# Kernel optimization log

Measured on AMD Instinct MI355X. Metric: run time of the kernel, lower is better.

## Reference

```python
import jax, jax.numpy as jnp
import numpy as np

D_K = 64
D_MODEL = 1024
N_HEADS = 16


def setup_inputs() -> dict:
    key = jax.random.key(0)
    ks = jax.random.split(key, 9)
    B, S = 2, 2048
    scale = 1.0 / np.sqrt(D_MODEL)
    inp = {
        "x": jax.random.normal(ks[0], (B, S, D_MODEL), dtype=jnp.float32),
        "w_q": jax.random.normal(ks[1], (D_MODEL, N_HEADS * D_K), dtype=jnp.float32) * scale,
        "b_q": jnp.zeros((N_HEADS * D_K,), dtype=jnp.float32),
        "w_k": jax.random.normal(ks[2], (D_MODEL, N_HEADS * D_K), dtype=jnp.float32) * scale,
        "b_k": jnp.zeros((N_HEADS * D_K,), dtype=jnp.float32),
        "w_v": jax.random.normal(ks[3], (D_MODEL, N_HEADS * D_K), dtype=jnp.float32) * scale,
        "b_v": jnp.zeros((N_HEADS * D_K,), dtype=jnp.float32),
        "w_o": jax.random.normal(ks[4], (N_HEADS * D_K, D_MODEL), dtype=jnp.float32) * scale,
        "b_o": jnp.zeros((D_MODEL,), dtype=jnp.float32),
    }
    return inp


def reference(x, w_q, b_q, w_k, b_k, w_v, b_v, w_o, b_o):
    B, S, _ = x.shape
    H, Dk = N_HEADS, D_K

    def split_heads(m):  # [B,S,H*Dk] -> [B,H,S,Dk]
        return m.reshape(B, S, H, Dk).transpose(0, 2, 1, 3)

    Q = split_heads(x @ w_q + b_q)
    K = split_heads(x @ w_k + b_k)
    V = split_heads(x @ w_v + b_v)

    scores = jnp.einsum("bhsd,bhtd->bhst", Q, K) / jnp.sqrt(jnp.float32(Dk))
    probs = jax.nn.softmax(scores, axis=-1)
    attn = jnp.einsum("bhst,bhtd->bhsd", probs, V)  # [B,H,S,Dk]
    attn = attn.transpose(0, 2, 1, 3).reshape(B, S, H * Dk)
    return attn @ w_o + b_o
```

## Files before the change

### kernel.cpp

```cpp
#include <hip/hip_runtime.h>
#include <math.h>

#define D_MODELc 1024
#define N_HEADSc 16
#define D_Kc     64
#define B_SZc    2
#define S_LENc   2048
#define NTOKc    (B_SZc * S_LENc)
#define SPLITc   4

using half8  = __attribute__((ext_vector_type(8))) _Float16;
using half4  = __attribute__((ext_vector_type(4))) _Float16;
using fp16x2 = __attribute__((ext_vector_type(2))) __fp16;
using float4v = __attribute__((ext_vector_type(4))) float;

__global__ __launch_bounds__(256) void cvt_all(
    const float* __restrict__ x,
    const float* __restrict__ W0, const float* __restrict__ W1,
    const float* __restrict__ W2, const float* __restrict__ W3,
    _Float16* __restrict__ wout, _Float16* __restrict__ xout)
{
    __shared__ float T[32][33];
    const int z = blockIdx.z;
    const int t = threadIdx.x;

    if (z == 4) {
        const int bid = blockIdx.y * 32 + blockIdx.x;
        #pragma unroll
        for (int c = 0; c < 2; ++c) {
            const int i = bid * 512 + c * 256 + t;
            float4v a = ((const float4v*)x)[2 * i];
            float4v b = ((const float4v*)x)[2 * i + 1];
            half8 h;
            h[0] = (_Float16)a[0]; h[1] = (_Float16)a[1];
            h[2] = (_Float16)a[2]; h[3] = (_Float16)a[3];
            h[4] = (_Float16)b[0]; h[5] = (_Float16)b[1];
            h[6] = (_Float16)b[2]; h[7] = (_Float16)b[3];
            ((half8*)xout)[i] = h;
        }
        return;
    }

    const float* W = (z == 0) ? W0 : (z == 1) ? W1 : (z == 2) ? W2 : W3;
    _Float16* O = wout + (size_t)z * 1024 * 1024;

    const int k0 = blockIdx.x * 32;
    const int n0 = blockIdx.y * 32;
    {
        const int r = t >> 3, c4 = (t & 7) * 4;
        float4v v = *(const float4v*)(W + (size_t)(k0 + r) * 1024 + n0 + c4);
        T[r][c4 + 0] = v[0]; T[r][c4 + 1] = v[1];
        T[r][c4 + 2] = v[2]; T[r][c4 + 3] = v[3];
    }
    __syncthreads();
    {
        const int rn = t >> 3, ck4 = (t & 7) * 4;
        half4 h;
        h[0] = (_Float16)T[ck4 + 0][rn];
        h[1] = (_Float16)T[ck4 + 1][rn];
        h[2] = (_Float16)T[ck4 + 2][rn];
        h[3] = (_Float16)T[ck4 + 3][rn];
        *(half4*)(O + (size_t)(n0 + rn) * 1024 + k0 + ck4) = h;
    }
}

__global__ __launch_bounds__(256) void gemm_qkv(
    const _Float16* __restrict__ A, const _Float16* __restrict__ BtAll,
    const float* __restrict__ bias0, const float* __restrict__ bias1,
    const float* __restrict__ bias2, _Float16* __restrict__ Cout)
{
    __shared__ _Float16 Als[2][128 * 32];
    __shared__ _Float16 Bls[2][128 * 32];

    constexpr int K = 1024;
    const int tid = threadIdx.x;
    const int m0  = blockIdx.x * 128;
    const int n0  = blockIdx.y * 128;
    const int z   = blockIdx.z;

    const _Float16* Bt  = BtAll + (size_t)z * 1024 * 1024;
    const float* bias   = (z == 0) ? bias0 : (z == 1) ? bias1 : bias2;
    const float qscale  = (z == 0) ? 0.18033688011112042f : 1.0f;

    const int wave = tid >> 6, lane = tid & 63;
    const int wr = wave >> 1, wc = wave & 1;
    const int quad = lane >> 4, l16 = lane & 15;

    float4v acc[4][4];
    #pragma unroll
    for (int i = 0; i < 4; ++i)
        #pragma unroll
        for (int j = 0; j < 4; ++j)
            acc[i][j] = (float4v){0.f, 0.f, 0.f, 0.f};

    for (int k0 = 0; k0 < K; k0 += 64) {
        #pragma unroll
        for (int c = 0; c < 2; ++c) {
            const int i   = c * 256 + tid;
            const int row = i >> 2, kc = i & 3;
            #pragma unroll
            for (int h = 0; h < 2; ++h) {
                __builtin_amdgcn_global_load_lds(
                    (const __attribute__((address_space(1))) void*)
                        (A + (size_t)(m0 + row) * K + k0 + h * 32 + kc * 8),
                    (__attribute__((address_space(3))) void*)(Als[h] + i * 8),
                    16, 0, 0);
                __builtin_amdgcn_global_load_lds(
                    (const __attribute__((address_space(1))) void*)
                        (Bt + (size_t)(n0 + row) * K + k0 + h * 32 + kc * 8),
                    (__attribute__((address_space(3))) void*)(Bls[h] + i * 8),
                    16, 0, 0);
            }
        }
        __syncthreads();

        half8 af[4][2], bf[4][2];
        #pragma unroll
        for (int i = 0; i < 4; ++i) {
            const int r = (wr * 64 + i * 16 + l16) * 32 + quad * 8;
            af[i][0] = *(const half8*)(Als[0] + r);
            af[i][1] = *(const half8*)(Als[1] + r);
        }
        #pragma unroll
        for (int j = 0; j < 4; ++j) {
            const int r = (wc * 64 + j * 16 + l16) * 32 + quad * 8;
            bf[j][0] = *(const half8*)(Bls[0] + r);
            bf[j][1] = *(const half8*)(Bls[1] + r);
        }
        #pragma unroll
        for (int i = 0; i < 4; ++i)
            #pragma unroll
            for (int j = 0; j < 4; ++j) {
                acc[i][j] = __builtin_amdgcn_mfma_f32_16x16x32_f16(
                    af[i][0], bf[j][0], acc[i][j], 0, 0, 0);
                acc[i][j] = __builtin_amdgcn_mfma_f32_16x16x32_f16(
                    af[i][1], bf[j][1], acc[i][j], 0, 0, 0);
            }
        __syncthreads();
    }

    if (z != 2) {
        #pragma unroll
        for (int i = 0; i < 4; ++i) {
            const int rbase = m0 + wr * 64 + i * 16 + quad * 4;
            #pragma unroll
            for (int j = 0; j < 4; ++j) {
                const int col = n0 + wc * 64 + j * 16 + l16;
                const float bv = bias[col];
                #pragma unroll
                for (int r = 0; r < 4; ++r) {
                    const float v = (acc[i][j][r] + bv) * qscale;
                    const int n = rbase + r;
                    const int b = n >> 11, s = n & 2047;
                    const int h = col >> 6, d = col & 63;
                    _Float16* C = Cout + (size_t)z * NTOKc * D_MODELc;
                    C[(((size_t)(b * N_HEADSc + h)) * S_LENc + s) * D_Kc + d] =
                        (_Float16)v;
                }
            }
        }
    } else {
        #pragma unroll
        for (int i = 0; i < 4; ++i) {
            const int rbase = m0 + wr * 64 + i * 16 + quad * 4;
            const int b = rbase >> 11, s0 = rbase & 2047;
            #pragma unroll
            for (int j = 0; j < 4; ++j) {
                const int col = n0 + wc * 64 + j * 16 + l16;
                const float bv = bias[col];
                const int h = col >> 6, d = col & 63;
                half4 hv;
                #pragma unroll
                for (int r = 0; r < 4; ++r)
                    hv[r] = (_Float16)(acc[i][j][r] + bv);
                _Float16* C = Cout + (size_t)2 * NTOKc * D_MODELc;
                *(half4*)(C + (((size_t)(b * N_HEADSc + h)) * D_Kc + d) *
                          S_LENc + s0) = hv;
            }
        }
    }
}

__global__ __launch_bounds__(256) void gemm_out(
    const _Float16* __restrict__ A, const _Float16* __restrict__ Bt,
    const float* __restrict__ bias, float* __restrict__ C)
{
    __shared__ _Float16 Als[2][64 * 32];
    __shared__ _Float16 Bls[2][128 * 32];

    constexpr int K = 1024;
    const int tid = threadIdx.x;
    const int m0  = blockIdx.x * 64;
    const int n0  = blockIdx.y * 128;

    const int wave = tid >> 6, lane = tid & 63;
    const int wr = wave >> 1, wc = wave & 1;
    const int quad = lane >> 4, l16 = lane & 15;

    float4v acc[2][4];
    #pragma unroll
    for (int i = 0; i < 2; ++i)
        #pragma unroll
        for (int j = 0; j < 4; ++j)
            acc[i][j] = (float4v){0.f, 0.f, 0.f, 0.f};

    for (int k0 = 0; k0 < K; k0 += 64) {
        {
            const int row = tid >> 2, kc = tid & 3;
            #pragma unroll
            for (int h = 0; h < 2; ++h)
                __builtin_amdgcn_global_load_lds(
                    (const __attribute__((address_space(1))) void*)
                        (A + (size_t)(m0 + row) * K + k0 + h * 32 + kc * 8),
                    (__attribute__((address_space(3))) void*)(Als[h] + tid * 8),
                    16, 0, 0);
        }
        #pragma unroll
        for (int c = 0; c < 2; ++c) {
            const int i = c * 256 + tid;
            const int row = i >> 2, kc = i & 3;
            #pragma unroll
            for (int h = 0; h < 2; ++h)
                __builtin_amdgcn_global_load_lds(
                    (const __attribute__((address_space(1))) void*)
                        (Bt + (size_t)(n0 + row) * K + k0 + h * 32 + kc * 8),
                    (__attribute__((address_space(3))) void*)(Bls[h] + i * 8),
                    16, 0, 0);
        }
        __syncthreads();

        half8 af[2][2], bf[4][2];
        #pragma unroll
        for (int i = 0; i < 2; ++i) {
            const int r = (wr * 32 + i * 16 + l16) * 32 + quad * 8;
            af[i][0] = *(const half8*)(Als[0] + r);
            af[i][1] = *(const half8*)(Als[1] + r);
        }
        #pragma unroll
        for (int j = 0; j < 4; ++j) {
            const int r = (wc * 64 + j * 16 + l16) * 32 + quad * 8;
            bf[j][0] = *(const half8*)(Bls[0] + r);
            bf[j][1] = *(const half8*)(Bls[1] + r);
        }
        #pragma unroll
        for (int i = 0; i < 2; ++i)
            #pragma unroll
            for (int j = 0; j < 4; ++j) {
                acc[i][j] = __builtin_amdgcn_mfma_f32_16x16x32_f16(
                    af[i][0], bf[j][0], acc[i][j], 0, 0, 0);
                acc[i][j] = __builtin_amdgcn_mfma_f32_16x16x32_f16(
                    af[i][1], bf[j][1], acc[i][j], 0, 0, 0);
            }
        __syncthreads();
    }

    #pragma unroll
    for (int i = 0; i < 2; ++i) {
        const int rbase = m0 + wr * 32 + i * 16 + quad * 4;
        #pragma unroll
        for (int j = 0; j < 4; ++j) {
            const int col = n0 + wc * 64 + j * 16 + l16;
            const float bv = bias[col];
            #pragma unroll
            for (int r = 0; r < 4; ++r)
                C[(size_t)(rbase + r) * 1024 + col] = acc[i][j][r] + bv;
        }
    }
}

__global__ __launch_bounds__(256) void attn_mfma(
    const _Float16* __restrict__ Qb, const _Float16* __restrict__ Kb,
    const _Float16* __restrict__ Vtg, _Float16* __restrict__ Op,
    float* __restrict__ Lp)
{
    constexpr int PS = 72;
    __shared__ _Float16 Ks[64 * PS];
    __shared__ _Float16 Vt[64 * PS];
    __shared__ _Float16 Ps[128 * PS];

    const int tid  = threadIdx.x;
    const int wv   = tid >> 6;
    const int lane = tid & 63;
    const int quad = lane >> 4;
    const int l16  = lane & 15;

    const int id  = blockIdx.x;
    const int cls = id & 7;
    const int idx = id >> 3;
    const int qi  = idx & 15;
    const int c0  = ((idx >> 4) << 3) | cls;
    const int bh  = c0 >> 2;
    const int sp  = c0 & 3;

    const int q0 = qi * 128;
    const int kb = sp * (S_LENc / SPLITc);
    const int kend = kb + S_LENc / SPLITc;

    const _Float16* Qsl = Qb  + (size_t)bh * S_LENc * D_Kc;
    const _Float16* Ksl = Kb  + (size_t)bh * S_LENc * D_Kc;
    const _Float16* Vsl = Vtg + (size_t)bh * S_LENc * D_Kc;

    half8 aq[2][2];
    #pragma unroll
    for (int qf = 0; qf < 2; ++qf) {
        const int row = q0 + wv * 32 + qf * 16 + l16;
        aq[qf][0] = *(const half8*)(Qsl + (size_t)row * 64 + quad * 8);
        aq[qf][1] = *(const half8*)(Qsl + (size_t)row * 64 + 32 + quad * 8);
    }

    float4v O[2][4];
    #pragma unroll
    for (int qf = 0; qf < 2; ++qf)
        #pragma unroll
        for (int nt = 0; nt < 4; ++nt)
            O[qf][nt] = (float4v){0.f, 0.f, 0.f, 0.f};
    float lr[2] = {0.f, 0.f};

    const int sr = tid >> 2;
    const int sg = (tid & 3) * 16;

    for (int t0 = kb; t0 < kend; t0 += 64) {
        half8 k0 = *(const half8*)(Ksl + (size_t)(t0 + sr) * 64 + sg);
        half8 k1 = *(const half8*)(Ksl + (size_t)(t0 + sr) * 64 + sg + 8);
        half8 v0 = *(const half8*)(Vsl + (size_t)sr * S_LENc + t0 + sg);
        half8 v1 = *(const half8*)(Vsl + (size_t)sr * S_LENc + t0 + sg + 8);
        __syncthreads();
        *(half8*)(Ks + sr * PS + sg)     = k0;
        *(half8*)(Ks + sr * PS + sg + 8) = k1;
        *(half8*)(Vt + sr * PS + sg)     = v0;
        *(half8*)(Vt + sr * PS + sg + 8) = v1;
        __syncthreads();

        half8 kf[4][2];
        #pragma unroll
        for (int nt = 0; nt < 4; ++nt) {
            kf[nt][0] = *(const half8*)(Ks + (nt * 16 + l16) * PS + quad * 8);
            kf[nt][1] = *(const half8*)(Ks + (nt * 16 + l16) * PS + 32 + quad * 8);
        }

        #pragma unroll
        for (int qf = 0; qf < 2; ++qf) {
            float4v st[4];
            #pragma unroll
            for (int nt = 0; nt < 4; ++nt) {
                st[nt] = __builtin_amdgcn_mfma_f32_16x16x32_f16(
                    kf[nt][0], aq[qf][0], (float4v){0.f, 0.f, 0.f, 0.f}, 0, 0, 0);
                st[nt] = __builtin_amdgcn_mfma_f32_16x16x32_f16(
                    kf[nt][1], aq[qf][1], st[nt], 0, 0, 0);
            }
            float ls = 0.f;
            #pragma unroll
            for (int nt = 0; nt < 4; ++nt) {
                const float p0 = __builtin_amdgcn_exp2f(fminf(st[nt][0], 15.5f));
                const float p1 = __builtin_amdgcn_exp2f(fminf(st[nt][1], 15.5f));
                const float p2 = __builtin_amdgcn_exp2f(fminf(st[nt][2], 15.5f));
                const float p3 = __builtin_amdgcn_exp2f(fminf(st[nt][3], 15.5f));
                ls += (p0 + p1) + (p2 + p3);
                union { fp16x2 h2[2]; half4 h4; } u;
                u.h2[0] = __builtin_amdgcn_cvt_pkrtz(p0, p1);
                u.h2[1] = __builtin_amdgcn_cvt_pkrtz(p2, p3);
                *(half4*)(Ps + (wv * 32 + qf * 16 + l16) * PS +
                          nt * 16 + quad * 4) = u.h4;
            }
            lr[qf] += ls;
        }

        half8 bvv[4][2];
        #pragma unroll
        for (int nt = 0; nt < 4; ++nt) {
            bvv[nt][0] = *(const half8*)(Vt + (nt * 16 + l16) * PS + quad * 8);
            bvv[nt][1] = *(const half8*)(Vt + (nt * 16 + l16) * PS + 32 + quad * 8);
        }
        #pragma unroll
        for (int qf = 0; qf < 2; ++qf) {
            half8 ap0 = *(const half8*)(Ps + (wv * 32 + qf * 16 + l16) * PS + quad * 8);
            half8 ap1 = *(const half8*)(Ps + (wv * 32 + qf * 16 + l16) * PS + 32 + quad * 8);
            #pragma unroll
            for (int nt = 0; nt < 4; ++nt) {
                O[qf][nt] = __builtin_amdgcn_mfma_f32_16x16x32_f16(
                    ap0, bvv[nt][0], O[qf][nt], 0, 0, 0);
                O[qf][nt] = __builtin_amdgcn_mfma_f32_16x16x32_f16(
                    ap1, bvv[nt][1], O[qf][nt], 0, 0, 0);
            }
        }
    }

    const size_t qgb = (size_t)bh * S_LENc;
    #pragma unroll
    for (int qf = 0; qf < 2; ++qf) {
        float t = lr[qf];
        t += __shfl_xor(t, 16, 64);
        t += __shfl_xor(t, 32, 64);
        if (quad == 0)
            Lp[(size_t)sp * 65536 + qgb + q0 + wv * 32 + qf * 16 + l16] = t;
        #pragma unroll
        for (int r = 0; r < 4; ++r) {
            const int q = q0 + wv * 32 + qf * 16 + quad * 4 + r;
            _Float16* dst = Op + ((size_t)sp * 65536 + qgb + q) * 64;
            #pragma unroll
            for (int nt = 0; nt < 4; ++nt)
                dst[nt * 16 + l16] = (_Float16)O[qf][nt][r];
        }
    }
}

__global__ __launch_bounds__(256) void attn_combine(
    const _Float16* __restrict__ Op, const float* __restrict__ Lp,
    _Float16* __restrict__ Ab)
{
    const int i  = blockIdx.x * 256 + threadIdx.x;
    const int e0 = i * 8;
    const int qg = e0 >> 6;
    const int d0 = e0 & 63;
    const int bh = qg >> 11, q = qg & 2047;
    const int b  = bh >> 4,  h = bh & 15;

    float lsum = 0.f;
    #pragma unroll
    for (int s = 0; s < SPLITc; ++s) lsum += Lp[(size_t)s * 65536 + qg];
    const float inv = 1.0f / lsum;

    float acc[8] = {};
    #pragma unroll
    for (int s = 0; s < SPLITc; ++s) {
        half8 o = *(const half8*)(Op + ((size_t)s * 65536 + qg) * 64 + d0);
        #pragma unroll
        for (int j = 0; j < 8; ++j) acc[j] += (float)o[j];
    }
    half8 hv;
    #pragma unroll
    for (int j = 0; j < 8; ++j) hv[j] = (_Float16)(acc[j] * inv);
    *(half8*)(Ab + ((size_t)(b * S_LENc + q)) * 1024 + h * 64 + d0) = hv;
}

extern "C" void kernel_launch(void* const* d_in, const int* in_sizes, int n_in,
                              void* d_out, int out_size, void* d_ws, size_t ws_size,
                              hipStream_t stream)
{
    const float* x  = (const float*)d_in[0];
    const float* wq = (const float*)d_in[1];
    const float* bq = (const float*)d_in[2];
    const float* wk = (const float*)d_in[3];
    const float* bk = (const float*)d_in[4];
    const float* wv = (const float*)d_in[5];
    const float* bv = (const float*)d_in[6];
    const float* wo = (const float*)d_in[7];
    const float* bo = (const float*)d_in[8];
    float* out = (float*)d_out;

    const size_t M1 = 1024 * 1024;
    const size_t M4 = 4 * M1;
    _Float16* xh = (_Float16*)d_ws;
    _Float16* wh = xh + M4;
    _Float16* Qh = wh + M4;
    _Float16* Oph = Qh + 3 * M4;
    float*    Lp  = (float*)(Oph + SPLITc * M4);
    _Float16* Ah = xh;

    cvt_all<<<dim3(32, 32, 5), dim3(256), 0, stream>>>(
        x, wq, wk, wv, wo, wh, xh);
    gemm_qkv<<<dim3(NTOKc / 128, D_MODELc / 128, 3), dim3(256), 0, stream>>>(
        xh, wh, bq, bk, bv, Qh);
    attn_mfma<<<dim3((S_LENc / 128) * B_SZc * N_HEADSc * SPLITc), dim3(256),
                0, stream>>>(
        Qh, Qh + M4, Qh + 2 * M4, Oph, Lp);
    attn_combine<<<dim3(NTOKc * D_MODELc / 8 / 256), dim3(256), 0, stream>>>(
        Oph, Lp, Ah);
    gemm_out<<<dim3(NTOKc / 64, D_MODELc / 128), dim3(256), 0, stream>>>(
        Ah, wh + 3 * M1, bo, out);
}
```

Baseline: 213.3 us.

## Keep attention probabilities in registers and halve the key split

The P matrix is no longer written to and reread from LDS. The exp'd scores stay in registers and feed a transposed 16x16x16 MFMA (V^T times P), which removes the Ps shared buffer and its LDS round trip. The key-dimension split drops from 4 to 2, so there are fewer partial outputs and the combine kernel does less work. Each partial is normalized in-kernel and the combine becomes a weighted average. The trade-off is fewer blocks in flight and more MFMA instructions of smaller shape, plus a possible register-pressure increase.

```diff
diff --git a/kernel.cpp b/kernel.cpp
--- a/kernel.cpp
+++ b/kernel.cpp
@@ -7,7 +7,7 @@
 #define B_SZc    2
 #define S_LENc   2048
 #define NTOKc    (B_SZc * S_LENc)
-#define SPLITc   4
+#define SPLITc   2
 
 using half8  = __attribute__((ext_vector_type(8))) _Float16;
 using half4  = __attribute__((ext_vector_type(4))) _Float16;
@@ -276,7 +276,6 @@
     constexpr int PS = 72;
     __shared__ _Float16 Ks[64 * PS];
     __shared__ _Float16 Vt[64 * PS];
-    __shared__ _Float16 Ps[128 * PS];
 
     const int tid  = threadIdx.x;
     const int wv   = tid >> 6;
@@ -289,8 +288,8 @@
     const int idx = id >> 3;
     const int qi  = idx & 15;
     const int c0  = ((idx >> 4) << 3) | cls;
-    const int bh  = c0 >> 2;
-    const int sp  = c0 & 3;
+    const int bh  = c0 >> 1;
+    const int sp  = c0 & 1;
 
     const int q0 = qi * 128;
     const int kb = sp * (S_LENc / SPLITc);
@@ -338,6 +337,7 @@
             kf[nt][1] = *(const half8*)(Ks + (nt * 16 + l16) * PS + 32 + quad * 8);
         }
 
+        half4 pb[2][4];
         #pragma unroll
         for (int qf = 0; qf < 2; ++qf) {
             float4v st[4];
@@ -359,29 +359,24 @@
                 union { fp16x2 h2[2]; half4 h4; } u;
                 u.h2[0] = __builtin_amdgcn_cvt_pkrtz(p0, p1);
                 u.h2[1] = __builtin_amdgcn_cvt_pkrtz(p2, p3);
-                *(half4*)(Ps + (wv * 32 + qf * 16 + l16) * PS +
-                          nt * 16 + quad * 4) = u.h4;
+                pb[qf][nt] = u.h4;
             }
             lr[qf] += ls;
         }
 
-        half8 bvv[4][2];
-        #pragma unroll
-        for (int nt = 0; nt < 4; ++nt) {
-            bvv[nt][0] = *(const half8*)(Vt + (nt * 16 + l16) * PS + quad * 8);
-            bvv[nt][1] = *(const half8*)(Vt + (nt * 16 + l16) * PS + 32 + quad * 8);
-        }
-        #pragma unroll
-        for (int qf = 0; qf < 2; ++qf) {
-            half8 ap0 = *(const half8*)(Ps + (wv * 32 + qf * 16 + l16) * PS + quad * 8);
-            half8 ap1 = *(const half8*)(Ps + (wv * 32 + qf * 16 + l16) * PS + 32 + quad * 8);
-            #pragma unroll
-            for (int nt = 0; nt < 4; ++nt) {
-                O[qf][nt] = __builtin_amdgcn_mfma_f32_16x16x32_f16(
-                    ap0, bvv[nt][0], O[qf][nt], 0, 0, 0);
-                O[qf][nt] = __builtin_amdgcn_mfma_f32_16x16x32_f16(
-                    ap1, bvv[nt][1], O[qf][nt], 0, 0, 0);
-            }
+        #pragma unroll
+        for (int ntd = 0; ntd < 4; ++ntd) {
+            half4 va[4];
+            #pragma unroll
+            for (int nt = 0; nt < 4; ++nt)
+                va[nt] = *(const half4*)(Vt + (ntd * 16 + l16) * PS +
+                                         nt * 16 + quad * 4);
+            #pragma unroll
+            for (int qf = 0; qf < 2; ++qf)
+                #pragma unroll
+                for (int nt = 0; nt < 4; ++nt)
+                    O[qf][ntd] = __builtin_amdgcn_mfma_f32_16x16x16f16(
+                        va[nt], pb[qf][nt], O[qf][ntd], 0, 0, 0);
         }
     }
 
@@ -391,15 +386,18 @@
         float t = lr[qf];
         t += __shfl_xor(t, 16, 64);
         t += __shfl_xor(t, 32, 64);
+        const float inv = 1.0f / t;
+        const int q = q0 + wv * 32 + qf * 16 + l16;
         if (quad == 0)
-            Lp[(size_t)sp * 65536 + qgb + q0 + wv * 32 + qf * 16 + l16] = t;
-        #pragma unroll
-        for (int r = 0; r < 4; ++r) {
-            const int q = q0 + wv * 32 + qf * 16 + quad * 4 + r;
-            _Float16* dst = Op + ((size_t)sp * 65536 + qgb + q) * 64;
-            #pragma unroll
-            for (int nt = 0; nt < 4; ++nt)
-                dst[nt * 16 + l16] = (_Float16)O[qf][nt][r];
+            Lp[(size_t)sp * 65536 + qgb + q] = t;
+        _Float16* dst = Op + ((size_t)sp * 65536 + qgb + q) * 64;
+        #pragma unroll
+        for (int ntd = 0; ntd < 4; ++ntd) {
+            half4 hv;
+            #pragma unroll
+            for (int r = 0; r < 4; ++r)
+                hv[r] = (_Float16)(O[qf][ntd][r] * inv);
+            *(half4*)(dst + ntd * 16 + quad * 4) = hv;
         }
     }
 }
@@ -415,21 +413,15 @@
     const int bh = qg >> 11, q = qg & 2047;
     const int b  = bh >> 4,  h = bh & 15;
 
-    float lsum = 0.f;
-    #pragma unroll
-    for (int s = 0; s < SPLITc; ++s) lsum += Lp[(size_t)s * 65536 + qg];
-    const float inv = 1.0f / lsum;
-
-    float acc[8] = {};
-    #pragma unroll
-    for (int s = 0; s < SPLITc; ++s) {
-        half8 o = *(const half8*)(Op + ((size_t)s * 65536 + qg) * 64 + d0);
-        #pragma unroll
-        for (int j = 0; j < 8; ++j) acc[j] += (float)o[j];
-    }
+    float l0 = Lp[qg], l1 = Lp[65536 + qg];
+    const float inv = 1.0f / (l0 + l1);
+    const float w0 = l0 * inv, w1 = l1 * inv;
+    half8 o0 = *(const half8*)(Op + (size_t)qg * 64 + d0);
+    half8 o1 = *(const half8*)(Op + ((size_t)65536 + qg) * 64 + d0);
     half8 hv;
     #pragma unroll
-    for (int j = 0; j < 8; ++j) hv[j] = (_Float16)(acc[j] * inv);
+    for (int j = 0; j < 8; ++j)
+        hv[j] = (_Float16)((float)o0[j] * w0 + (float)o1[j] * w1);
     *(half8*)(Ab + ((size_t)(b * S_LENc + q)) * 1024 + h * 64 + d0) = hv;
 }
 
```

Measured after the change: 209.0 us. 1.02x faster.
